# Kernel tuning notes

Hardware: AMD Instinct MI355X
Metric: run time of the kernel (lower is better)

The kernel has to match this reference:

```python
import jax, jax.numpy as jnp
import numpy as np

B, C, H, W = 8, 256, 48, 48
G = 32  # num_groups
EPS = 1e-5


def setup_inputs() -> dict:
    key = jax.random.key(0)
    ks = jax.random.split(key, 9)
    s = 0.02
    return {
        "input": jax.random.normal(ks[0], (B, C, H, W), dtype=jnp.float32),
        "Wq": jax.random.normal(ks[1], (C, C), dtype=jnp.float32) * s,
        "bq": jnp.zeros((C,), dtype=jnp.float32),
        "Wk": jax.random.normal(ks[2], (C, C), dtype=jnp.float32) * s,
        "bk": jnp.zeros((C,), dtype=jnp.float32),
        "Wv": jax.random.normal(ks[3], (C, C), dtype=jnp.float32) * s,
        "bv": jnp.zeros((C,), dtype=jnp.float32),
        "gn_w": jnp.ones((C,), dtype=jnp.float32),
        "gn_b": jnp.zeros((C,), dtype=jnp.float32),
    }


def _group_norm(x, w, b):
    # x: [B, C, H, W] -> normalize per (group) over (C//G, H, W)
    n, c, h, wd = x.shape
    xg = x.reshape(n, G, c // G, h, wd)
    mean = jnp.mean(xg, axis=(2, 3, 4), keepdims=True)
    var = jnp.var(xg, axis=(2, 3, 4), keepdims=True)
    xg = (xg - mean) * jax.lax.rsqrt(var + EPS)
    x = xg.reshape(n, c, h, wd)
    return x * w[None, :, None, None] + b[None, :, None, None]


def _conv1x1(x, wgt, bias):
    # 1x1 conv == per-pixel channel GEMM. wgt: [C_out, C_in]
    return jnp.einsum('bchw,oc->bohw', x, wgt) + bias[None, :, None, None]


def reference(input, Wq, bq, Wk, bk, Wv, bv, gn_w, gn_b):
    x = _group_norm(input, gn_w, gn_b)
    q = _conv1x1(x, Wq, bq)
    k = _conv1x1(x, Wk, bk)
    v = _conv1x1(x, Wv, bv)
    d = q.shape[1]
    # energy[b,h,w,h',w'] = sum_c q[b,c,h,w] * k[b,c,h',w'] / sqrt(d)
    energy = jnp.einsum('bchw,bcef->bhwef', q, k) / jnp.sqrt(jnp.float32(d))
    n, h, w2 = energy.shape[0], energy.shape[1], energy.shape[2]
    energy = jax.nn.softmax(energy.reshape(n, h, w2, h * w2), axis=-1)
    energy = energy.reshape(n, h, w2, h, w2)
    # out[b,c,h,w] = sum_{h',w'} energy[b,h,w,h',w'] * v[b,c,h',w']
    out = jnp.einsum('bhwef,bcef->bchw', energy, v)
    return out
```

## Files before the change

### kernel.cpp

```cpp
#include <hip/hip_runtime.h>
#include <math.h>

#define NB 8
#define NC 256
#define NHW 2304
#define NG 32
#define CPG 8
#define GN_EPS 1e-5f
#define ATT_SCALE 0.0625f
#define XSTR 258

typedef __bf16 bf16x8 __attribute__((ext_vector_type(8)));
typedef __bf16 bf16x4 __attribute__((ext_vector_type(4)));
typedef float f32x4 __attribute__((ext_vector_type(4)));

#define MFMA(a, b, c) __builtin_amdgcn_mfma_f32_16x16x32_bf16(a, b, c, 0, 0, 0)

__device__ __forceinline__ void async_lds16(const void* g, void* l) {
  __builtin_amdgcn_global_load_lds(
      (const __attribute__((address_space(1))) void*)g,
      (__attribute__((address_space(3))) void*)l, 16, 0, 0);
}

__global__ __launch_bounds__(256) void k_prep(
    const float* __restrict__ x, const float* __restrict__ gn_w,
    const float* __restrict__ gn_b, float* __restrict__ scale,
    float* __restrict__ shift,
    const float* __restrict__ Wq, const float* __restrict__ Wk,
    const float* __restrict__ Wv, __bf16* __restrict__ Wqb,
    __bf16* __restrict__ Wkb, __bf16* __restrict__ Wvb) {
  __shared__ float red[8];
  int blk = blockIdx.x;
  if (blk >= 256) {
    int idx = blk - 256;
    int which = idx >> 6;
    const float* src = which == 0 ? Wq : (which == 1 ? Wk : Wv);
    __bf16* dst = which == 0 ? Wqb : (which == 1 ? Wkb : Wvb);
    int i = (idx & 63) * 256 + threadIdx.x;
    float4 v = ((const float4*)src)[i];
    bf16x4 o;
    o[0] = (__bf16)v.x; o[1] = (__bf16)v.y;
    o[2] = (__bf16)v.z; o[3] = (__bf16)v.w;
    ((bf16x4*)dst)[i] = o;
    return;
  }
  const float4* base = (const float4*)(x + (size_t)blk * CPG * NHW);
  const int n4 = CPG * NHW / 4;
  float s = 0.f, ss = 0.f;
  for (int i = threadIdx.x; i < n4; i += 256) {
    float4 v = base[i];
    s  += v.x + v.y + v.z + v.w;
    ss += v.x * v.x + v.y * v.y + v.z * v.z + v.w * v.w;
  }
  for (int off = 32; off > 0; off >>= 1) {
    s  += __shfl_down(s, off);
    ss += __shfl_down(ss, off);
  }
  int wv = threadIdx.x >> 6, ln = threadIdx.x & 63;
  if (ln == 0) { red[wv] = s; red[4 + wv] = ss; }
  __syncthreads();
  if (threadIdx.x < CPG) {
    float S  = red[0] + red[1] + red[2] + red[3];
    float SS = red[4] + red[5] + red[6] + red[7];
    const float inv_n = 1.f / (float)(CPG * NHW);
    float mean = S * inv_n;
    float var  = SS * inv_n - mean * mean;
    float rstd = rsqrtf(var + GN_EPS);
    int b = blk / NG, g = blk % NG;
    int c = g * CPG + threadIdx.x;
    float sc = gn_w[c] * rstd;
    scale[b * NC + c] = sc;
    shift[b * NC + c] = gn_b[c] - mean * sc;
  }
}

__global__ __launch_bounds__(256) void k_xnT(
    const float* __restrict__ x, const float* __restrict__ scale,
    const float* __restrict__ shift, __bf16* __restrict__ xnT) {
  __shared__ __bf16 t[64 * XSTR];
  int p0 = blockIdx.x * 64;
  int b = blockIdx.y;
  int w = threadIdx.x >> 6, lane = threadIdx.x & 63;
  const float* xb = x + (size_t)b * NC * NHW;
  const float* scb = scale + b * NC;
  const float* shb = shift + b * NC;
#pragma unroll 8
  for (int i = 0; i < 64; ++i) {
    int c = i * 4 + w;
    float v = xb[(size_t)c * NHW + p0 + lane] * scb[c] + shb[c];
    t[lane * XSTR + c] = (__bf16)v;
  }
  __syncthreads();
#pragma unroll
  for (int i = 0; i < 8; ++i) {
    int row = i * 8 + w * 2 + (lane >> 5);
    int c8 = (lane & 31) * 8;
    bf16x8 v8 = *(const bf16x8*)&t[row * XSTR + c8];
    *(bf16x8*)&xnT[((size_t)b * NHW + p0 + row) * NC + c8] = v8;
  }
}

__global__ __launch_bounds__(256) void k_qkv(
    const __bf16* __restrict__ xnT,
    const __bf16* __restrict__ Wqb, const __bf16* __restrict__ Wkb,
    const __bf16* __restrict__ Wvb,
    const float* __restrict__ bq, const float* __restrict__ bk,
    const float* __restrict__ bv,
    __bf16* __restrict__ qT, __bf16* __restrict__ kT,
    __bf16* __restrict__ vbuf) {
  __shared__ __bf16 tile[9216];
  int blk = blockIdx.x;
  int b = blk & 7;
  int r = blk >> 3;
  int oq = r & 3;
  int pg = r >> 2;
  int p0 = pg * 128, o0 = oq * 64;
  int tid = threadIdx.x;
  int w = tid >> 6, lane = tid & 63;
  int col = lane & 15, quad = lane >> 4;

  const __bf16* xrow =
      xnT + ((size_t)b * NHW + p0 + w * 32 + col) * NC + quad * 8;
  bf16x8 xf[2][8];
#pragma unroll
  for (int mt = 0; mt < 2; ++mt)
#pragma unroll
    for (int ks = 0; ks < 8; ++ks)
      xf[mt][ks] = *(const bf16x8*)(xrow + (size_t)mt * 16 * NC + ks * 32);

#pragma unroll
  for (int t = 0; t < 3; ++t) {
    const __bf16* W = t == 0 ? Wqb : (t == 1 ? Wkb : Wvb);
    const float* bias = t == 0 ? bq : (t == 1 ? bk : bv);
    f32x4 acc[2][4];
#pragma unroll
    for (int mt = 0; mt < 2; ++mt)
#pragma unroll
      for (int nt = 0; nt < 4; ++nt) acc[mt][nt] = (f32x4){0.f, 0.f, 0.f, 0.f};
#pragma unroll
    for (int nt = 0; nt < 4; ++nt) {
      const __bf16* wrow = W + ((size_t)(o0 + nt * 16 + col)) * NC + quad * 8;
#pragma unroll
      for (int ks = 0; ks < 8; ++ks) {
        bf16x8 wf = *(const bf16x8*)(wrow + ks * 32);
        acc[0][nt] = MFMA(xf[0][ks], wf, acc[0][nt]);
        acc[1][nt] = MFMA(xf[1][ks], wf, acc[1][nt]);
      }
    }
    if (t > 0) __syncthreads();
    if (t < 2) {
#pragma unroll
      for (int mt = 0; mt < 2; ++mt)
#pragma unroll
        for (int nt = 0; nt < 4; ++nt) {
          float bc = bias[o0 + nt * 16 + col];
#pragma unroll
          for (int reg = 0; reg < 4; ++reg) {
            int row = w * 32 + mt * 16 + quad * 4 + reg;
            tile[row * 72 + nt * 16 + col] = (__bf16)(acc[mt][nt][reg] + bc);
          }
        }
      __syncthreads();
      __bf16* dst = t == 0 ? qT : kT;
#pragma unroll
      for (int pass = 0; pass < 4; ++pass) {
        int unit = pass * 256 + tid;
        int row = unit >> 3, ch = unit & 7;
        bf16x8 v8 = *(const bf16x8*)&tile[row * 72 + ch * 8];
        *(bf16x8*)&dst[((size_t)b * NHW + p0 + row) * NC + o0 + ch * 8] = v8;
      }
    } else {
#pragma unroll
      for (int mt = 0; mt < 2; ++mt)
#pragma unroll
        for (int nt = 0; nt < 4; ++nt) {
          float bc = bias[o0 + nt * 16 + col];
#pragma unroll
          for (int reg = 0; reg < 4; ++reg) {
            int p = w * 32 + mt * 16 + quad * 4 + reg;
            tile[(nt * 16 + col) * 136 + p] = (__bf16)(acc[mt][nt][reg] + bc);
          }
        }
      __syncthreads();
#pragma unroll
      for (int pass = 0; pass < 4; ++pass) {
        int unit = pass * 256 + tid;
        int row = unit >> 4, ch = unit & 15;
        bf16x8 v8 = *(const bf16x8*)&tile[row * 136 + ch * 8];
        *(bf16x8*)&vbuf[((size_t)b * NC + o0 + row) * NHW + p0 + ch * 8] = v8;
      }
    }
  }
}

__global__ __launch_bounds__(256, 3) void k_sexp(
    const __bf16* __restrict__ qT, const __bf16* __restrict__ kT,
    __bf16* __restrict__ P, float* __restrict__ lsum) {
  __shared__ __bf16 sk[64 * 256];
  __bf16* pt = sk;
  int blk = blockIdx.x;
  int b = blk & 7;
  int r = blk >> 3;
  int kt = r % 36;
  int qg = r / 36;
  int q0 = qg * 128, k0 = kt * 64;
  int tid = threadIdx.x;
  int w = tid >> 6, lane = tid & 63;
  int col = lane & 15, quad = lane >> 4;

  {
    int sub = lane >> 5;
    int p5 = lane & 31;
#pragma unroll
    for (int j = 0; j < 8; ++j) {
      int r0 = w * 16 + j * 2;
      int rloc = r0 + sub;
      int g = p5 ^ (rloc & 7);
      const __bf16* gp = kT + ((size_t)b * NHW + k0 + rloc) * NC + g * 8;
      async_lds16(gp, (void*)&sk[r0 * 256]);
    }
  }
  const __bf16* qrow =
      qT + ((size_t)b * NHW + q0 + w * 32 + col) * NC + quad * 8;
  bf16x8 qf[2][8];
#pragma unroll
  for (int mt = 0; mt < 2; ++mt)
#pragma unroll
    for (int ks = 0; ks < 8; ++ks)
      qf[mt][ks] = *(const bf16x8*)(qrow + (size_t)mt * 16 * NC + ks * 32);
  __syncthreads();

  f32x4 sacc[2][4];
#pragma unroll
  for (int mt = 0; mt < 2; ++mt)
#pragma unroll
    for (int nt = 0; nt < 4; ++nt) sacc[mt][nt] = (f32x4){0.f, 0.f, 0.f, 0.f};
  int c7 = col & 7;
#pragma unroll
  for (int nt = 0; nt < 4; ++nt) {
    int rrow = nt * 16 + col;
#pragma unroll
    for (int ks = 0; ks < 8; ++ks) {
      int c = ks * 4 + quad;
      bf16x8 kf = *(const bf16x8*)&sk[rrow * 256 + ((c ^ c7) << 3)];
      sacc[0][nt] = MFMA(qf[0][ks], kf, sacc[0][nt]);
      sacc[1][nt] = MFMA(qf[1][ks], kf, sacc[1][nt]);
    }
  }
#pragma unroll
  for (int mt = 0; mt < 2; ++mt)
#pragma unroll
    for (int reg = 0; reg < 4; ++reg) {
      float rs = 0.f;
#pragma unroll
      for (int nt = 0; nt < 4; ++nt) {
        float e = __expf(sacc[mt][nt][reg] * ATT_SCALE);
        sacc[mt][nt][reg] = e;
        rs += e;
      }
      rs += __shfl_xor(rs, 1);
      rs += __shfl_xor(rs, 2);
      rs += __shfl_xor(rs, 4);
      rs += __shfl_xor(rs, 8);
      if (col == 0) {
        int row = w * 32 + mt * 16 + quad * 4 + reg;
        atomicAdd(&lsum[(size_t)b * NHW + q0 + row], rs);
      }
    }
  __syncthreads();
#pragma unroll
  for (int mt = 0; mt < 2; ++mt)
#pragma unroll
    for (int nt = 0; nt < 4; ++nt)
#pragma unroll
      for (int reg = 0; reg < 4; ++reg) {
        int row = w * 32 + mt * 16 + quad * 4 + reg;
        pt[row * 72 + nt * 16 + col] = (__bf16)sacc[mt][nt][reg];
      }
  __syncthreads();
#pragma unroll
  for (int pass = 0; pass < 4; ++pass) {
    int unit = pass * 256 + tid;
    int row = unit >> 3, ch = unit & 7;
    bf16x8 v8 = *(const bf16x8*)&pt[row * 72 + ch * 8];
    *(bf16x8*)&P[((size_t)b * NHW + q0 + row) * NHW + k0 + ch * 8] = v8;
  }
}

__global__ __launch_bounds__(256, 4) void k_pv(
    const __bf16* __restrict__ P, const __bf16* __restrict__ vbuf,
    const float* __restrict__ lsum, float* __restrict__ out) {
  __shared__ __bf16 sp[3][144 * 64];
  int blk = blockIdx.x;
  int b = blk & 7;
  int r = blk >> 3;
  int cq = r & 3;
  int qg = r >> 2;
  int q0 = qg * 144;
  int tid = threadIdx.x;
  int w = tid >> 6, lane = tid & 63;
  int col = lane & 15, quad = lane >> 4;
  int c0 = cq * 64 + w * 16;

  int sub = lane >> 3;
  int gsw = (lane & 7) ^ (sub & 7);
  const __bf16* pbase = P + ((size_t)b * NHW + q0) * NHW;

  f32x4 acc[9];
#pragma unroll
  for (int nt = 0; nt < 9; ++nt) acc[nt] = (f32x4){0.f, 0.f, 0.f, 0.f};

  const __bf16* vbase =
      vbuf + ((size_t)b * NC + c0 + col) * NHW + quad * 8;
  int c7 = col & 7;

  for (int j = w; j < 18; j += 4) {
    const __bf16* gp = pbase + (size_t)(j * 8 + sub) * NHW + gsw * 8;
    async_lds16(gp, (void*)&sp[0][j * 512]);
  }
  for (int it = 0; it < 36; ++it) {
    const __bf16* buf = sp[it % 3];
    if (it < 35) {
      __bf16* nbuf = sp[(it + 1) % 3];
      const __bf16* pn = pbase + (size_t)(it + 1) * 64;
      for (int j = w; j < 18; j += 4) {
        const __bf16* gp = pn + (size_t)(j * 8 + sub) * NHW + gsw * 8;
        async_lds16(gp, (void*)&nbuf[j * 512]);
      }
      if (w < 2)
        asm volatile("s_waitcnt vmcnt(5)\n\ts_barrier" ::: "memory");
      else
        asm volatile("s_waitcnt vmcnt(4)\n\ts_barrier" ::: "memory");
    } else {
      asm volatile("s_waitcnt vmcnt(0)\n\ts_barrier" ::: "memory");
    }
    const __bf16* vp = vbase + it * 64;
#pragma unroll
    for (int ks = 0; ks < 2; ++ks) {
      bf16x8 vf = *(const bf16x8*)(vp + ks * 32);
      int c = ks * 4 + quad;
#pragma unroll
      for (int nt = 0; nt < 9; ++nt) {
        int row = nt * 16 + col;
        bf16x8 pf = *(const bf16x8*)&buf[row * 64 + ((c ^ c7) << 3)];
        acc[nt] = MFMA(vf, pf, acc[nt]);
      }
    }
  }
  float* ob = out + (size_t)b * NC * NHW;
#pragma unroll
  for (int nt = 0; nt < 9; ++nt) {
    float inv = 1.f / lsum[(size_t)b * NHW + q0 + nt * 16 + col];
#pragma unroll
    for (int reg = 0; reg < 4; ++reg) {
      int c = c0 + quad * 4 + reg;
      ob[(size_t)c * NHW + q0 + nt * 16 + col] = acc[nt][reg] * inv;
    }
  }
}

extern "C" void kernel_launch(void* const* d_in, const int* in_sizes, int n_in,
                              void* d_out, int out_size, void* d_ws,
                              size_t ws_size, hipStream_t stream) {
  const float* x   = (const float*)d_in[0];
  const float* Wq  = (const float*)d_in[1];
  const float* bq  = (const float*)d_in[2];
  const float* Wk  = (const float*)d_in[3];
  const float* bk  = (const float*)d_in[4];
  const float* Wv  = (const float*)d_in[5];
  const float* bv  = (const float*)d_in[6];
  const float* gnw = (const float*)d_in[7];
  const float* gnb = (const float*)d_in[8];
  float* out = (float*)d_out;

  const size_t per = (size_t)NB * NC * NHW;
  const size_t psz = (size_t)NB * NHW * NHW * 2;
  char* wsb = (char*)d_ws;
  __bf16* qT   = (__bf16*)wsb;
  __bf16* kT   = (__bf16*)(wsb + per * 2);
  __bf16* vbuf = (__bf16*)(wsb + per * 4);
  __bf16* xnT  = (__bf16*)(wsb + per * 6);
  __bf16* P    = (__bf16*)(wsb + per * 6);
  char* tail   = wsb + per * 6 + psz;
  __bf16* Wqb  = (__bf16*)tail;
  __bf16* Wkb  = Wqb + NC * NC;
  __bf16* Wvb  = Wkb + NC * NC;
  float* scale = (float*)(Wvb + NC * NC);
  float* shift = scale + NB * NC;
  float* lsum  = shift + NB * NC;

  hipMemsetAsync(lsum, 0, (size_t)NB * NHW * sizeof(float), stream);
  hipLaunchKernelGGL(k_prep, dim3(448), dim3(256), 0, stream,
                     x, gnw, gnb, scale, shift, Wq, Wk, Wv, Wqb, Wkb, Wvb);
  hipLaunchKernelGGL(k_xnT, dim3(NHW / 64, NB), dim3(256), 0, stream,
                     x, scale, shift, xnT);
  hipLaunchKernelGGL(k_qkv, dim3(576), dim3(256), 0, stream,
                     xnT, Wqb, Wkb, Wvb, bq, bk, bv, qT, kT, vbuf);
  hipLaunchKernelGGL(k_sexp, dim3(5184), dim3(256), 0, stream,
                     qT, kT, P, lsum);
  hipLaunchKernelGGL(k_pv, dim3(512), dim3(256), 0, stream,
                     P, vbuf, lsum, out);
}
```

Measured before the change: 234.4 us.

## Fuse score-exp and PV kernels into a flash-style attention kernel

Replaces the separate QK^T/exp kernel and the P·V kernel with one fused kernel. Each block owns 64 queries and loops over 36 key tiles, staging K and V into LDS, computing exp scores, writing bf16 probabilities to a small LDS tile, and accumulating P·V in registers. Row sums stay in registers and LDS, so the global lsum atomics and memset go away. The aim is to stop writing and reading back the full bf16 probability matrix through HBM. The cost is a small grid of only 288 blocks, which may leave many CUs underused, plus barrier-heavy single-buffered staging.

```diff
diff --git a/kernel.cpp b/kernel.cpp
--- a/kernel.cpp
+++ b/kernel.cpp
@@ -193,168 +193,162 @@
   }
 }
 
-__global__ __launch_bounds__(256, 3) void k_sexp(
+__global__ __launch_bounds__(256, 2) void k_fused(
     const __bf16* __restrict__ qT, const __bf16* __restrict__ kT,
-    __bf16* __restrict__ P, float* __restrict__ lsum) {
+    const __bf16* __restrict__ vbuf, float* __restrict__ out) {
   __shared__ __bf16 sk[64 * 256];
-  __bf16* pt = sk;
+  __shared__ __bf16 sv[256 * 64];
+  __shared__ __bf16 sp[64 * 64];
+  __shared__ float slsum[2][64];
+
   int blk = blockIdx.x;
   int b = blk & 7;
-  int r = blk >> 3;
-  int kt = r % 36;
-  int qg = r / 36;
-  int q0 = qg * 128, k0 = kt * 64;
+  int qg = blk >> 3;
+  int q0 = qg * 64;
   int tid = threadIdx.x;
   int w = tid >> 6, lane = tid & 63;
+  int wm = w >> 1, wn = w & 1;
   int col = lane & 15, quad = lane >> 4;
-
-  {
-    int sub = lane >> 5;
-    int p5 = lane & 31;
-#pragma unroll
-    for (int j = 0; j < 8; ++j) {
-      int r0 = w * 16 + j * 2;
-      int rloc = r0 + sub;
-      int g = p5 ^ (rloc & 7);
-      const __bf16* gp = kT + ((size_t)b * NHW + k0 + rloc) * NC + g * 8;
-      async_lds16(gp, (void*)&sk[r0 * 256]);
-    }
-  }
+  int c7 = col & 7;
+
+  auto stage_kv = [&](int it2) {
+    int k0 = it2 * 64;
+    {
+      int sub = lane >> 5, p5 = lane & 31;
+#pragma unroll
+      for (int j = 0; j < 8; ++j) {
+        int r0 = w * 16 + j * 2;
+        int rloc = r0 + sub;
+        int g = p5 ^ (rloc & 7);
+        async_lds16(kT + ((size_t)b * NHW + k0 + rloc) * NC + g * 8,
+                    (void*)&sk[r0 * 256]);
+      }
+    }
+    {
+      int sub = lane >> 3, p3 = lane & 7;
+#pragma unroll
+      for (int j = 0; j < 8; ++j) {
+        int r0 = w * 64 + j * 8;
+        int rloc = r0 + sub;
+        int g = p3 ^ (rloc & 7);
+        async_lds16(vbuf + ((size_t)b * NC + rloc) * NHW + k0 + g * 8,
+                    (void*)&sv[r0 * 64]);
+      }
+    }
+  };
+
   const __bf16* qrow =
-      qT + ((size_t)b * NHW + q0 + w * 32 + col) * NC + quad * 8;
+      qT + ((size_t)b * NHW + q0 + wn * 32 + col) * NC + quad * 8;
   bf16x8 qf[2][8];
 #pragma unroll
-  for (int mt = 0; mt < 2; ++mt)
+  for (int nt = 0; nt < 2; ++nt)
 #pragma unroll
     for (int ks = 0; ks < 8; ++ks)
-      qf[mt][ks] = *(const bf16x8*)(qrow + (size_t)mt * 16 * NC + ks * 32);
+      qf[nt][ks] = *(const bf16x8*)(qrow + (size_t)nt * 16 * NC + ks * 32);
+
+  stage_kv(0);
+
+  f32x4 acc[4][4];
+#pragma unroll
+  for (int mt = 0; mt < 4; ++mt)
+#pragma unroll
+    for (int nt = 0; nt < 4; ++nt) acc[mt][nt] = (f32x4){0.f, 0.f, 0.f, 0.f};
+  float lsum_r[2] = {0.f, 0.f};
+
+  for (int it = 0; it < 36; ++it) {
+    __syncthreads();
+
+    f32x4 sacc[2][2];
+#pragma unroll
+    for (int mt = 0; mt < 2; ++mt)
+#pragma unroll
+      for (int nt = 0; nt < 2; ++nt) sacc[mt][nt] = (f32x4){0.f, 0.f, 0.f, 0.f};
+#pragma unroll
+    for (int ks = 0; ks < 8; ++ks) {
+#pragma unroll
+      for (int mt = 0; mt < 2; ++mt) {
+        int krow = wm * 32 + mt * 16 + col;
+        bf16x8 kf = *(const bf16x8*)
+            &sk[krow * 256 + (((ks * 4 + quad) ^ c7) << 3)];
+        sacc[mt][0] = MFMA(kf, qf[0][ks], sacc[mt][0]);
+        sacc[mt][1] = MFMA(kf, qf[1][ks], sacc[mt][1]);
+      }
+    }
+
+#pragma unroll
+    for (int nt = 0; nt < 2; ++nt) {
+      float ps = 0.f;
+      int q = wn * 32 + nt * 16 + col;
+#pragma unroll
+      for (int mt = 0; mt < 2; ++mt) {
+        bf16x4 pk;
+#pragma unroll
+        for (int reg = 0; reg < 4; ++reg) {
+          float e = __expf(sacc[mt][nt][reg] * ATT_SCALE);
+          ps += e;
+          pk[reg] = (__bf16)e;
+        }
+        int chunk = (wm * 4 + mt * 2 + (quad >> 1)) ^ c7;
+        *(bf16x4*)&sp[q * 64 + chunk * 8 + (quad & 1) * 4] = pk;
+      }
+      ps += __shfl_xor(ps, 16);
+      ps += __shfl_xor(ps, 32);
+      lsum_r[nt] += ps;
+    }
+
+    __syncthreads();
+
+    bf16x8 pf[4][2], vf[4][2];
+#pragma unroll
+    for (int nt = 0; nt < 4; ++nt) {
+      int q = nt * 16 + col;
+#pragma unroll
+      for (int ks = 0; ks < 2; ++ks)
+        pf[nt][ks] = *(const bf16x8*)
+            &sp[q * 64 + (((ks * 4 + quad) ^ c7) << 3)];
+    }
+#pragma unroll
+    for (int mt = 0; mt < 4; ++mt) {
+      int crow = w * 64 + mt * 16 + col;
+#pragma unroll
+      for (int ks = 0; ks < 2; ++ks)
+        vf[mt][ks] = *(const bf16x8*)
+            &sv[crow * 64 + (((ks * 4 + quad) ^ c7) << 3)];
+    }
+    if (it < 35) {
+      asm volatile("s_waitcnt lgkmcnt(0)" ::: "memory");
+      __builtin_amdgcn_sched_barrier(0);
+      stage_kv(it + 1);
+    }
+
+#pragma unroll
+    for (int mt = 0; mt < 4; ++mt)
+#pragma unroll
+      for (int nt = 0; nt < 4; ++nt) {
+        acc[mt][nt] = MFMA(vf[mt][0], pf[nt][0], acc[mt][nt]);
+        acc[mt][nt] = MFMA(vf[mt][1], pf[nt][1], acc[mt][nt]);
+      }
+  }
+
+  if (quad == 0) {
+#pragma unroll
+    for (int nt = 0; nt < 2; ++nt)
+      slsum[wm][wn * 32 + nt * 16 + col] = lsum_r[nt];
+  }
   __syncthreads();
 
-  f32x4 sacc[2][4];
-#pragma unroll
-  for (int mt = 0; mt < 2; ++mt)
-#pragma unroll
-    for (int nt = 0; nt < 4; ++nt) sacc[mt][nt] = (f32x4){0.f, 0.f, 0.f, 0.f};
-  int c7 = col & 7;
+  float* ob = out + (size_t)b * NC * NHW;
 #pragma unroll
   for (int nt = 0; nt < 4; ++nt) {
-    int rrow = nt * 16 + col;
-#pragma unroll
-    for (int ks = 0; ks < 8; ++ks) {
-      int c = ks * 4 + quad;
-      bf16x8 kf = *(const bf16x8*)&sk[rrow * 256 + ((c ^ c7) << 3)];
-      sacc[0][nt] = MFMA(qf[0][ks], kf, sacc[0][nt]);
-      sacc[1][nt] = MFMA(qf[1][ks], kf, sacc[1][nt]);
-    }
-  }
-#pragma unroll
-  for (int mt = 0; mt < 2; ++mt)
-#pragma unroll
-    for (int reg = 0; reg < 4; ++reg) {
-      float rs = 0.f;
-#pragma unroll
-      for (int nt = 0; nt < 4; ++nt) {
-        float e = __expf(sacc[mt][nt][reg] * ATT_SCALE);
-        sacc[mt][nt][reg] = e;
-        rs += e;
-      }
-      rs += __shfl_xor(rs, 1);
-      rs += __shfl_xor(rs, 2);
-      rs += __shfl_xor(rs, 4);
-      rs += __shfl_xor(rs, 8);
-      if (col == 0) {
-        int row = w * 32 + mt * 16 + quad * 4 + reg;
-        atomicAdd(&lsum[(size_t)b * NHW + q0 + row], rs);
-      }
-    }
-  __syncthreads();
-#pragma unroll
-  for (int mt = 0; mt < 2; ++mt)
-#pragma unroll
-    for (int nt = 0; nt < 4; ++nt)
+    int q = nt * 16 + col;
+    float inv = 1.f / (slsum[0][q] + slsum[1][q]);
+#pragma unroll
+    for (int mt = 0; mt < 4; ++mt) {
 #pragma unroll
       for (int reg = 0; reg < 4; ++reg) {
-        int row = w * 32 + mt * 16 + quad * 4 + reg;
-        pt[row * 72 + nt * 16 + col] = (__bf16)sacc[mt][nt][reg];
-      }
-  __syncthreads();
-#pragma unroll
-  for (int pass = 0; pass < 4; ++pass) {
-    int unit = pass * 256 + tid;
-    int row = unit >> 3, ch = unit & 7;
-    bf16x8 v8 = *(const bf16x8*)&pt[row * 72 + ch * 8];
-    *(bf16x8*)&P[((size_t)b * NHW + q0 + row) * NHW + k0 + ch * 8] = v8;
-  }
-}
-
-__global__ __launch_bounds__(256, 4) void k_pv(
-    const __bf16* __restrict__ P, const __bf16* __restrict__ vbuf,
-    const float* __restrict__ lsum, float* __restrict__ out) {
-  __shared__ __bf16 sp[3][144 * 64];
-  int blk = blockIdx.x;
-  int b = blk & 7;
-  int r = blk >> 3;
-  int cq = r & 3;
-  int qg = r >> 2;
-  int q0 = qg * 144;
-  int tid = threadIdx.x;
-  int w = tid >> 6, lane = tid & 63;
-  int col = lane & 15, quad = lane >> 4;
-  int c0 = cq * 64 + w * 16;
-
-  int sub = lane >> 3;
-  int gsw = (lane & 7) ^ (sub & 7);
-  const __bf16* pbase = P + ((size_t)b * NHW + q0) * NHW;
-
-  f32x4 acc[9];
-#pragma unroll
-  for (int nt = 0; nt < 9; ++nt) acc[nt] = (f32x4){0.f, 0.f, 0.f, 0.f};
-
-  const __bf16* vbase =
-      vbuf + ((size_t)b * NC + c0 + col) * NHW + quad * 8;
-  int c7 = col & 7;
-
-  for (int j = w; j < 18; j += 4) {
-    const __bf16* gp = pbase + (size_t)(j * 8 + sub) * NHW + gsw * 8;
-    async_lds16(gp, (void*)&sp[0][j * 512]);
-  }
-  for (int it = 0; it < 36; ++it) {
-    const __bf16* buf = sp[it % 3];
-    if (it < 35) {
-      __bf16* nbuf = sp[(it + 1) % 3];
-      const __bf16* pn = pbase + (size_t)(it + 1) * 64;
-      for (int j = w; j < 18; j += 4) {
-        const __bf16* gp = pn + (size_t)(j * 8 + sub) * NHW + gsw * 8;
-        async_lds16(gp, (void*)&nbuf[j * 512]);
-      }
-      if (w < 2)
-        asm volatile("s_waitcnt vmcnt(5)\n\ts_barrier" ::: "memory");
-      else
-        asm volatile("s_waitcnt vmcnt(4)\n\ts_barrier" ::: "memory");
-    } else {
-      asm volatile("s_waitcnt vmcnt(0)\n\ts_barrier" ::: "memory");
-    }
-    const __bf16* vp = vbase + it * 64;
-#pragma unroll
-    for (int ks = 0; ks < 2; ++ks) {
-      bf16x8 vf = *(const bf16x8*)(vp + ks * 32);
-      int c = ks * 4 + quad;
-#pragma unroll
-      for (int nt = 0; nt < 9; ++nt) {
-        int row = nt * 16 + col;
-        bf16x8 pf = *(const bf16x8*)&buf[row * 64 + ((c ^ c7) << 3)];
-        acc[nt] = MFMA(vf, pf, acc[nt]);
-      }
-    }
-  }
-  float* ob = out + (size_t)b * NC * NHW;
-#pragma unroll
-  for (int nt = 0; nt < 9; ++nt) {
-    float inv = 1.f / lsum[(size_t)b * NHW + q0 + nt * 16 + col];
-#pragma unroll
-    for (int reg = 0; reg < 4; ++reg) {
-      int c = c0 + quad * 4 + reg;
-      ob[(size_t)c * NHW + q0 + nt * 16 + col] = acc[nt][reg] * inv;
+        int c = w * 64 + mt * 16 + quad * 4 + reg;
+        ob[(size_t)c * NHW + q0 + q] = acc[mt][nt][reg] * inv;
+      }
     }
   }
 }
@@ -380,24 +374,19 @@
   __bf16* kT   = (__bf16*)(wsb + per * 2);
   __bf16* vbuf = (__bf16*)(wsb + per * 4);
   __bf16* xnT  = (__bf16*)(wsb + per * 6);
-  __bf16* P    = (__bf16*)(wsb + per * 6);
   char* tail   = wsb + per * 6 + psz;
   __bf16* Wqb  = (__bf16*)tail;
   __bf16* Wkb  = Wqb + NC * NC;
   __bf16* Wvb  = Wkb + NC * NC;
   float* scale = (float*)(Wvb + NC * NC);
   float* shift = scale + NB * NC;
-  float* lsum  = shift + NB * NC;
-
-  hipMemsetAsync(lsum, 0, (size_t)NB * NHW * sizeof(float), stream);
+
   hipLaunchKernelGGL(k_prep, dim3(448), dim3(256), 0, stream,
                      x, gnw, gnb, scale, shift, Wq, Wk, Wv, Wqb, Wkb, Wvb);
   hipLaunchKernelGGL(k_xnT, dim3(NHW / 64, NB), dim3(256), 0, stream,
                      x, scale, shift, xnT);
   hipLaunchKernelGGL(k_qkv, dim3(576), dim3(256), 0, stream,
                      xnT, Wqb, Wkb, Wvb, bq, bk, bv, qT, kT, vbuf);
-  hipLaunchKernelGGL(k_sexp, dim3(5184), dim3(256), 0, stream,
-                     qT, kT, P, lsum);
-  hipLaunchKernelGGL(k_pv, dim3(512), dim3(256), 0, stream,
-                     P, vbuf, lsum, out);
-}
+  hipLaunchKernelGGL(k_fused, dim3(288), dim3(256), 0, stream,
+                     qT, kT, vbuf, out);
+}
```

After: 243.6 us. +3.9%, slower.
